# Kernel optimization log

Measured on AMD Instinct MI355X. Metric: run time of the kernel, lower is better.

The kernel has to match this reference:

```python
import jax, jax.numpy as jnp
import numpy as np

B, N, D, DC, R = 32, 36, 2048, 4, 512  # batch, regions, feat dim, coord dim, fusion rank


def setup_inputs() -> dict:
    key = jax.random.key(0)
    ks = jax.random.split(key, 8)
    s = lambda fan_in: 1.0 / np.sqrt(fan_in)
    return {
        "mm": jax.random.normal(ks[0], (B, N, D), dtype=jnp.float32),
        "coords": jax.random.uniform(ks[1], (B, N, DC), dtype=jnp.float32),
        "U_feat": jax.random.normal(ks[2], (D, R), dtype=jnp.float32) * s(D),
        "V_feat": jax.random.normal(ks[3], (D, R), dtype=jnp.float32) * s(D),
        "P_feat": jax.random.normal(ks[4], (R, D), dtype=jnp.float32) * s(R),
        "U_coord": jax.random.normal(ks[5], (DC, R), dtype=jnp.float32) * s(DC),
        "V_coord": jax.random.normal(ks[6], (DC, R), dtype=jnp.float32) * s(DC),
        "P_coord": jax.random.normal(ks[7], (R, D), dtype=jnp.float32) * s(R),
    }


def reference(mm, coords, U_feat, V_feat, P_feat, U_coord, V_coord, P_coord):
    # Pairwise module: build all (i, j) region pairs, fuse, max-aggregate over j.
    # Original torch code detach_()'s the gathered pair tensors -> stop_gradient here.
    mm_sg = jax.lax.stop_gradient(mm)
    coords_sg = jax.lax.stop_gradient(coords)

    # Coord fusion (MLB-style low-rank multiplicative fusion)
    uc = jnp.einsum("bnc,cr->bnr", coords_sg, U_coord)   # [B,N,R]
    vc = jnp.einsum("bnc,cr->bnr", coords_sg, V_coord)   # [B,N,R]
    zc = jax.nn.relu(uc[:, :, None, :] * vc[:, None, :, :])  # [B,N,N,R]
    Rij = jnp.einsum("bijr,rd->bijd", zc, P_coord)       # [B,N,N,D]

    # Feature fusion
    uf = jnp.einsum("bnd,dr->bnr", mm_sg, U_feat)
    vf = jnp.einsum("bnd,dr->bnr", mm_sg, V_feat)
    zf = jax.nn.relu(uf[:, :, None, :] * vf[:, None, :, :])  # [B,N,N,R]
    Rij = Rij + jnp.einsum("bijr,rd->bijd", zf, P_feat)  # [B,N,N,D]

    # agg['type'] == 'max': reduce over the second region axis (j)
    mm_new = jnp.max(Rij, axis=2)                        # [B,N,D]

    # residual
    return mm_new + mm
```

## Files before the change

### kernel.cpp

```cpp
#include <hip/hip_runtime.h>

#define BI    1152
#define NREG  36
#define DD    2048
#define RR    512
#define KK    1024
#define ZROWS (BI*NREG)
#define MBLK  144
#define NBLK  256
#define ABUF  (MBLK*32)
#define BBUF  (NBLK*32)
#define BUFE  (ABUF+BBUF)

typedef __bf16 bf16;
typedef __bf16 bf16x8 __attribute__((ext_vector_type(8)));
typedef __bf16 bf16x4 __attribute__((ext_vector_type(4)));
typedef float  f32x4  __attribute__((ext_vector_type(4)));

__device__ __forceinline__ void gl_lds16(const void* g, void* l) {
  __builtin_amdgcn_global_load_lds(
      (const __attribute__((address_space(1))) unsigned int*)g,
      (__attribute__((address_space(3))) unsigned int*)l, 16, 0, 0);
}

__global__ void k_prep(const float* __restrict__ mm, const float* __restrict__ coords,
                       const float* __restrict__ U_feat, const float* __restrict__ V_feat,
                       const float* __restrict__ P_feat, const float* __restrict__ U_coord,
                       const float* __restrict__ V_coord, const float* __restrict__ P_coord,
                       bf16* __restrict__ mmb, bf16* __restrict__ UT, bf16* __restrict__ VT,
                       bf16* __restrict__ PTt, float* __restrict__ uc, float* __restrict__ vc) {
  __shared__ float tile[32][33];
  int bid = blockIdx.x, tid = threadIdx.x;
  if (bid < 2304) {
    int i = bid * 256 + tid;
    float4 v = ((const float4*)mm)[i];
    bf16x4 o = {(bf16)v.x, (bf16)v.y, (bf16)v.z, (bf16)v.w};
    ((bf16x4*)mmb)[i] = o;
  } else if (bid < 4352) {
    int rel = bid - 2304;
    int zz = rel >> 10, rr = rel & 1023;
    int c0 = (rr & 15) * 32, r0 = (rr >> 4) * 32;
    const float* in = zz ? V_feat : U_feat;
    bf16* outp = zz ? VT : UT;
    int tx = tid & 31, ty = tid >> 5;
#pragma unroll
    for (int k = 0; k < 4; k++)
      tile[ty + 8 * k][tx] = in[(long)(r0 + ty + 8 * k) * 512 + c0 + tx];
    __syncthreads();
#pragma unroll
    for (int k = 0; k < 4; k++)
      outp[(long)(c0 + ty + 8 * k) * 2048 + r0 + tx] = (bf16)tile[tx][ty + 8 * k];
  } else if (bid < 6400) {
    int rel = bid - 4352;
    int zz = rel >> 10, rr = rel & 1023;
    int c0 = (rr & 63) * 32, r0 = (rr >> 6) * 32;
    const float* in = zz ? P_feat : P_coord;
    int koff = zz * 512;
    int tx = tid & 31, ty = tid >> 5;
#pragma unroll
    for (int k = 0; k < 4; k++)
      tile[ty + 8 * k][tx] = in[(long)(r0 + ty + 8 * k) * 2048 + c0 + tx];
    __syncthreads();
    int kc = (koff + r0) >> 5;
#pragma unroll
    for (int k = 0; k < 4; k++) {
      int d = c0 + ty + 8 * k;
      PTt[((long)kc * 2048 + d) * 32 + tx] = (bf16)tile[tx][ty + 8 * k];
    }
  } else {
    int g = bid - 6400;
    float c0 = coords[g * 4 + 0], c1 = coords[g * 4 + 1];
    float c2 = coords[g * 4 + 2], c3 = coords[g * 4 + 3];
#pragma unroll
    for (int i = 0; i < 2; i++) {
      int r = tid + i * 256;
      uc[g * RR + r] = c0 * U_coord[r] + c1 * U_coord[RR + r] + c2 * U_coord[2 * RR + r] + c3 * U_coord[3 * RR + r];
      vc[g * RR + r] = c0 * V_coord[r] + c1 * V_coord[RR + r] + c2 * V_coord[2 * RR + r] + c3 * V_coord[3 * RR + r];
    }
  }
}

__launch_bounds__(256)
__global__ void k_gemm_uv(const bf16* __restrict__ mmb, const bf16* __restrict__ UT,
                          const bf16* __restrict__ VT, float* __restrict__ uf,
                          float* __restrict__ vf, float* __restrict__ uf2,
                          float* __restrict__ vf2) {
  __shared__ bf16 lds2[2][6144];
  int uv = blockIdx.z >> 1, kh = blockIdx.z & 1;
  const bf16* Bmat = uv ? VT : UT;
  float* outp = uv ? (kh ? vf2 : vf) : (kh ? uf2 : uf);
  int m0 = blockIdx.x * 64, n0 = blockIdx.y * 128;
  int kbase = kh * 1024;
  int tid = threadIdx.x, wave = tid >> 6, lane = tid & 63;
  int l15 = lane & 15, qv = lane >> 4;
  int qp_c = qv ^ ((l15 >> 1) & 3);
  int qs = (lane & 3) ^ ((lane >> 3) & 3);

  const bf16* gA = mmb + (long)(m0 + wave * 16 + (lane >> 2)) * 2048 + kbase + qs * 8;
  const bf16* gB = Bmat + (long)(n0 + wave * 32 + (lane >> 2)) * 2048 + kbase + qs * 8;
  int lA = wave * 512;
  int lB = 2048 + wave * 1024;

  auto stage = [&](int buf, int k0) {
    bf16* db = &lds2[buf][0];
    gl_lds16(gA + k0, db + lA);
    gl_lds16(gB + k0, db + lB);
    gl_lds16(gB + 16 * 2048 + k0, db + lB + 512);
  };

  f32x4 acc[4][2] = {};
  stage(0, 0);
  for (int k0 = 0; k0 < 1024; k0 += 32) {
    int cur = (k0 >> 5) & 1;
    __syncthreads();
    if (k0 + 32 < 1024) stage(cur ^ 1, k0 + 32);
    bf16x8 a[4], b[2];
#pragma unroll
    for (int mt = 0; mt < 4; mt++)
      a[mt] = *(const bf16x8*)(&lds2[cur][0] + (mt * 16 + l15) * 32 + qp_c * 8);
#pragma unroll
    for (int nt = 0; nt < 2; nt++)
      b[nt] = *(const bf16x8*)(&lds2[cur][2048] + (wave * 32 + nt * 16 + l15) * 32 + qp_c * 8);
#pragma unroll
    for (int mt = 0; mt < 4; mt++)
#pragma unroll
      for (int nt = 0; nt < 2; nt++)
        acc[mt][nt] = __builtin_amdgcn_mfma_f32_16x16x32_bf16(a[mt], b[nt], acc[mt][nt], 0, 0, 0);
  }
#pragma unroll
  for (int mt = 0; mt < 4; mt++)
#pragma unroll
    for (int nt = 0; nt < 2; nt++)
#pragma unroll
      for (int r = 0; r < 4; r++) {
        int row = m0 + mt * 16 + qv * 4 + r;
        int col = n0 + wave * 32 + nt * 16 + l15;
        outp[(long)row * RR + col] = acc[mt][nt][r];
      }
}

__global__ void k_build_z(const float* __restrict__ uc, const float* __restrict__ vc,
                          const float* __restrict__ uf, const float* __restrict__ vf,
                          const float* __restrict__ uf2, const float* __restrict__ vf2,
                          bf16* __restrict__ z) {
  __shared__ float uL[36 * 128];
  __shared__ float vL[36 * 128];
  int kq = blockIdx.x, b = blockIdx.y, tid = threadIdx.x;
  int kb = (kq & 3) * 128;
  for (int i = tid; i < 1152; i += 256) {
    int row = i >> 5, kk = (i & 31) * 4;
    long src = (long)(b * 36 + row) * RR + kb + kk;
    float4 u4, v4;
    if (kq < 4) {
      u4 = *(const float4*)(uc + src);
      v4 = *(const float4*)(vc + src);
    } else {
      float4 a1 = *(const float4*)(uf + src), a2 = *(const float4*)(uf2 + src);
      float4 b1 = *(const float4*)(vf + src), b2 = *(const float4*)(vf2 + src);
      u4.x = a1.x + a2.x; u4.y = a1.y + a2.y; u4.z = a1.z + a2.z; u4.w = a1.w + a2.w;
      v4.x = b1.x + b2.x; v4.y = b1.y + b2.y; v4.z = b1.z + b2.z; v4.w = b1.w + b2.w;
    }
    *(float4*)&uL[row * 128 + kk] = u4;
    *(float4*)&vL[row * 128 + kk] = v4;
  }
  __syncthreads();
  int cbase = blockIdx.z * 20736;
  for (int c = cbase + tid; c < cbase + 20736; c += 256) {
    int kcl = c / 10368;
    int rem = c - kcl * 10368;
    int row = rem >> 3;
    int x4 = rem & 7;
    int gl = row / 36;
    int j = row - gl * 36;
    int kl = kcl * 32 + x4 * 4;
    float4 u4 = *(const float4*)&uL[gl * 128 + kl];
    float4 v4 = *(const float4*)&vL[j * 128 + kl];
    float x0 = fmaxf(u4.x * v4.x, 0.f), x1 = fmaxf(u4.y * v4.y, 0.f);
    float x2 = fmaxf(u4.z * v4.z, 0.f), x3 = fmaxf(u4.w * v4.w, 0.f);
    bf16x4 o = {(bf16)x0, (bf16)x1, (bf16)x2, (bf16)x3};
    int bi = b * 36 + gl;
    long rowp = (long)(bi >> 2) * 144 + j * 4 + (bi & 3);
    *(bf16x4*)(z + ((long)(kq * 4 + kcl) * ZROWS + rowp) * 32 + x4 * 4) = o;
  }
}

__launch_bounds__(256, 2)
__global__ void k_main(const bf16* __restrict__ z, const bf16* __restrict__ PTt,
                       const float* __restrict__ mm, float* __restrict__ out) {
  __shared__ bf16 lds[2 * BUFE];
  int bid = blockIdx.x;
  int x = bid & 7, t = bid >> 3;
  int dt = t & 7, go = (t >> 3) * 8 + x;
  int d0 = dt * NBLK;
  int tid = threadIdx.x, wave = tid >> 6, lane = tid & 63;
  int l15 = lane & 15, qv = lane >> 4;
  int qp_c = qv ^ ((l15 >> 1) & 3);
  int qs = (lane & 3) ^ ((lane >> 3) & 3);
  int lroff = (lane >> 2) * 32 + qs * 8;

  const bf16* gA = z + (long)go * ABUF + wave * 1024 + lroff;
  const bf16* gB = PTt + (long)d0 * 32 + wave * 2048 + lroff;
  int lA = wave * 1024;
  int lB = ABUF + wave * 2048;

  int sbuf = 0;
  auto stage = [&]() {
    bf16* db = lds + sbuf * BUFE;
    gl_lds16(gA, db + lA);
    gl_lds16(gA + 512, db + lA + 512);
    if (wave == 0) gl_lds16(gA + 4096, db + 4096);
    gl_lds16(gB, db + lB);
    gl_lds16(gB + 512, db + lB + 512);
    gl_lds16(gB + 1024, db + lB + 1024);
    gl_lds16(gB + 1536, db + lB + 1536);
    gA += (long)ZROWS * 32;
    gB += 2048L * 32;
    sbuf ^= 1;
  };

  f32x4 acc[9][4] = {};
  stage();
  for (int kc = 0; kc < 32; kc++) {
    __syncthreads();
    if (kc < 31) stage();
    const bf16* cur = lds + (kc & 1) * BUFE;
    bf16x8 b[4];
#pragma unroll
    for (int nt = 0; nt < 4; nt++)
      b[nt] = *(const bf16x8*)(cur + ABUF + (wave * 64 + nt * 16 + l15) * 32 + qp_c * 8);
#pragma unroll
    for (int mt = 0; mt < 9; mt++) {
      bf16x8 av = *(const bf16x8*)(cur + (mt * 16 + l15) * 32 + qp_c * 8);
#pragma unroll
      for (int nt = 0; nt < 4; nt++)
        acc[mt][nt] = __builtin_amdgcn_mfma_f32_16x16x32_bf16(av, b[nt], acc[mt][nt], 0, 0, 0);
    }
  }

#pragma unroll
  for (int nt = 0; nt < 4; nt++) {
    float mx[4];
#pragma unroll
    for (int r = 0; r < 4; r++) {
      mx[r] = acc[0][nt][r];
#pragma unroll
      for (int mt = 1; mt < 9; mt++) mx[r] = fmaxf(mx[r], acc[mt][nt][r]);
      mx[r] = fmaxf(mx[r], __shfl_xor(mx[r], 16, 64));
      mx[r] = fmaxf(mx[r], __shfl_xor(mx[r], 32, 64));
    }
    if (lane < 16) {
      int col = d0 + wave * 64 + nt * 16 + lane;
#pragma unroll
      for (int r = 0; r < 4; r++) {
        long oa = (long)(go * 4 + r) * DD + col;
        out[oa] = mx[r] + mm[oa];
      }
    }
  }
}

extern "C" void kernel_launch(void* const* d_in, const int* in_sizes, int n_in,
                              void* d_out, int out_size, void* d_ws, size_t ws_size,
                              hipStream_t stream) {
  const float* mm     = (const float*)d_in[0];
  const float* coords = (const float*)d_in[1];
  const float* U_feat = (const float*)d_in[2];
  const float* V_feat = (const float*)d_in[3];
  const float* P_feat = (const float*)d_in[4];
  const float* U_coord= (const float*)d_in[5];
  const float* V_coord= (const float*)d_in[6];
  const float* P_coord= (const float*)d_in[7];
  float* out = (float*)d_out;

  char* ws = (char*)d_ws;
  bf16* z   = (bf16*)(ws + 0);
  bf16* PTt = (bf16*)(ws + 84934656);
  bf16* mmb = (bf16*)(ws + 89128960);
  bf16* UT  = (bf16*)(ws + 93847552);
  bf16* VT  = (bf16*)(ws + 95944704);
  float* uf = (float*)(ws + 98041856);
  float* vf = (float*)(ws + 100401152);
  float* uc = (float*)(ws + 102760448);
  float* vc = (float*)(ws + 105119744);
  float* uf2= (float*)(ws + 107479040);
  float* vf2= (float*)(ws + 109838336);

  k_prep<<<dim3(7552), dim3(256), 0, stream>>>(mm, coords, U_feat, V_feat, P_feat,
                                               U_coord, V_coord, P_coord,
                                               mmb, UT, VT, PTt, uc, vc);
  k_gemm_uv<<<dim3(18, 4, 4), dim3(256), 0, stream>>>(mmb, UT, VT, uf, vf, uf2, vf2);
  k_build_z<<<dim3(8, 32, 2), dim3(256), 0, stream>>>(uc, vc, uf, vf, uf2, vf2, z);
  k_main<<<dim3(2304), dim3(256), 0, stream>>>(z, PTt, mm, out);
}
```

Baseline: 247.4 us.

## Triple-buffer main GEMM pipeline with explicit vmcnt waits and split uv GEMM 4-way

Changes the main fused GEMM from double to triple buffering in LDS, prefetching two K-chunks ahead. It replaces __syncthreads with manual s_waitcnt vmcnt plus s_barrier so one stage of loads stays in flight during compute. It also raises the split-K of the uv projection GEMM from 2 to 4 for more parallelism, summing the four partials in the z-building kernel. The cost is more LDS per block, which may limit occupancy, and extra partial-sum traffic.

```diff
diff --git a/kernel.cpp b/kernel.cpp
--- a/kernel.cpp
+++ b/kernel.cpp
@@ -82,15 +82,14 @@
 
 __launch_bounds__(256)
 __global__ void k_gemm_uv(const bf16* __restrict__ mmb, const bf16* __restrict__ UT,
-                          const bf16* __restrict__ VT, float* __restrict__ uf,
-                          float* __restrict__ vf, float* __restrict__ uf2,
-                          float* __restrict__ vf2) {
+                          const bf16* __restrict__ VT, float* __restrict__ ufp,
+                          float* __restrict__ vfp) {
   __shared__ bf16 lds2[2][6144];
-  int uv = blockIdx.z >> 1, kh = blockIdx.z & 1;
+  int uv = blockIdx.z >> 2, kh = blockIdx.z & 3;
   const bf16* Bmat = uv ? VT : UT;
-  float* outp = uv ? (kh ? vf2 : vf) : (kh ? uf2 : uf);
+  float* outp = (uv ? vfp : ufp) + (long)kh * (BI * RR);
   int m0 = blockIdx.x * 64, n0 = blockIdx.y * 128;
-  int kbase = kh * 1024;
+  int kbase = kh * 512;
   int tid = threadIdx.x, wave = tid >> 6, lane = tid & 63;
   int l15 = lane & 15, qv = lane >> 4;
   int qp_c = qv ^ ((l15 >> 1) & 3);
@@ -110,10 +109,10 @@
 
   f32x4 acc[4][2] = {};
   stage(0, 0);
-  for (int k0 = 0; k0 < 1024; k0 += 32) {
+  for (int k0 = 0; k0 < 512; k0 += 32) {
     int cur = (k0 >> 5) & 1;
     __syncthreads();
-    if (k0 + 32 < 1024) stage(cur ^ 1, k0 + 32);
+    if (k0 + 32 < 512) stage(cur ^ 1, k0 + 32);
     bf16x8 a[4], b[2];
 #pragma unroll
     for (int mt = 0; mt < 4; mt++)
@@ -140,8 +139,7 @@
 }
 
 __global__ void k_build_z(const float* __restrict__ uc, const float* __restrict__ vc,
-                          const float* __restrict__ uf, const float* __restrict__ vf,
-                          const float* __restrict__ uf2, const float* __restrict__ vf2,
+                          const float* __restrict__ ufp, const float* __restrict__ vfp,
                           bf16* __restrict__ z) {
   __shared__ float uL[36 * 128];
   __shared__ float vL[36 * 128];
@@ -155,10 +153,15 @@
       u4 = *(const float4*)(uc + src);
       v4 = *(const float4*)(vc + src);
     } else {
-      float4 a1 = *(const float4*)(uf + src), a2 = *(const float4*)(uf2 + src);
-      float4 b1 = *(const float4*)(vf + src), b2 = *(const float4*)(vf2 + src);
-      u4.x = a1.x + a2.x; u4.y = a1.y + a2.y; u4.z = a1.z + a2.z; u4.w = a1.w + a2.w;
-      v4.x = b1.x + b2.x; v4.y = b1.y + b2.y; v4.z = b1.z + b2.z; v4.w = b1.w + b2.w;
+      u4 = make_float4(0.f, 0.f, 0.f, 0.f);
+      v4 = make_float4(0.f, 0.f, 0.f, 0.f);
+#pragma unroll
+      for (int p = 0; p < 4; p++) {
+        float4 a1 = *(const float4*)(ufp + (long)p * (BI * RR) + src);
+        float4 b1 = *(const float4*)(vfp + (long)p * (BI * RR) + src);
+        u4.x += a1.x; u4.y += a1.y; u4.z += a1.z; u4.w += a1.w;
+        v4.x += b1.x; v4.y += b1.y; v4.z += b1.z; v4.w += b1.w;
+      }
     }
     *(float4*)&uL[row * 128 + kk] = u4;
     *(float4*)&vL[row * 128 + kk] = v4;
@@ -187,7 +190,7 @@
 __launch_bounds__(256, 2)
 __global__ void k_main(const bf16* __restrict__ z, const bf16* __restrict__ PTt,
                        const float* __restrict__ mm, float* __restrict__ out) {
-  __shared__ bf16 lds[2 * BUFE];
+  __shared__ bf16 lds[3 * BUFE];
   int bid = blockIdx.x;
   int x = bid & 7, t = bid >> 3;
   int dt = t & 7, go = (t >> 3) * 8 + x;
@@ -203,27 +206,35 @@
   int lA = wave * 1024;
   int lB = ABUF + wave * 2048;
 
-  int sbuf = 0;
-  auto stage = [&]() {
-    bf16* db = lds + sbuf * BUFE;
-    gl_lds16(gA, db + lA);
-    gl_lds16(gA + 512, db + lA + 512);
-    if (wave == 0) gl_lds16(gA + 4096, db + 4096);
-    gl_lds16(gB, db + lB);
-    gl_lds16(gB + 512, db + lB + 512);
-    gl_lds16(gB + 1024, db + lB + 1024);
-    gl_lds16(gB + 1536, db + lB + 1536);
-    gA += (long)ZROWS * 32;
-    gB += 2048L * 32;
-    sbuf ^= 1;
+  auto stage = [&](int buf, int kc) {
+    bf16* db = lds + buf * BUFE;
+    long ka = (long)kc * (ZROWS * 32L);
+    long kb = (long)kc * (2048L * 32);
+    gl_lds16(gA + ka, db + lA);
+    gl_lds16(gA + ka + 512, db + lA + 512);
+    if (wave == 3) gl_lds16(gA + ka + 1024, db + lA + 1024);
+    gl_lds16(gB + kb, db + lB);
+    gl_lds16(gB + kb + 512, db + lB + 512);
+    gl_lds16(gB + kb + 1024, db + lB + 1024);
+    gl_lds16(gB + kb + 1536, db + lB + 1536);
   };
 
   f32x4 acc[9][4] = {};
-  stage();
+  stage(0, 0);
+  stage(1, 1);
+  int buf = 0;
   for (int kc = 0; kc < 32; kc++) {
-    __syncthreads();
-    if (kc < 31) stage();
-    const bf16* cur = lds + (kc & 1) * BUFE;
+    if (kc < 31) {
+      if (wave == 3) __asm__ volatile("s_waitcnt vmcnt(7)\n\ts_barrier" ::: "memory");
+      else           __asm__ volatile("s_waitcnt vmcnt(6)\n\ts_barrier" ::: "memory");
+    } else {
+      __asm__ volatile("s_waitcnt vmcnt(0)\n\ts_barrier" ::: "memory");
+    }
+    if (kc + 2 < 32) {
+      int bnext = buf + 2; if (bnext >= 3) bnext -= 3;
+      stage(bnext, kc + 2);
+    }
+    const bf16* cur = lds + buf * BUFE;
     bf16x8 b[4];
 #pragma unroll
     for (int nt = 0; nt < 4; nt++)
@@ -235,6 +246,7 @@
       for (int nt = 0; nt < 4; nt++)
         acc[mt][nt] = __builtin_amdgcn_mfma_f32_16x16x32_bf16(av, b[nt], acc[mt][nt], 0, 0, 0);
     }
+    buf++; if (buf >= 3) buf -= 3;
   }
 
 #pragma unroll
@@ -278,17 +290,15 @@
   bf16* mmb = (bf16*)(ws + 89128960);
   bf16* UT  = (bf16*)(ws + 93847552);
   bf16* VT  = (bf16*)(ws + 95944704);
-  float* uf = (float*)(ws + 98041856);
-  float* vf = (float*)(ws + 100401152);
-  float* uc = (float*)(ws + 102760448);
-  float* vc = (float*)(ws + 105119744);
-  float* uf2= (float*)(ws + 107479040);
-  float* vf2= (float*)(ws + 109838336);
+  float* ufp= (float*)(ws + 98041856);
+  float* vfp= (float*)(ws + 107479040);
+  float* uc = (float*)(ws + 116916224);
+  float* vc = (float*)(ws + 119275520);
 
   k_prep<<<dim3(7552), dim3(256), 0, stream>>>(mm, coords, U_feat, V_feat, P_feat,
                                                U_coord, V_coord, P_coord,
                                                mmb, UT, VT, PTt, uc, vc);
-  k_gemm_uv<<<dim3(18, 4, 4), dim3(256), 0, stream>>>(mmb, UT, VT, uf, vf, uf2, vf2);
-  k_build_z<<<dim3(8, 32, 2), dim3(256), 0, stream>>>(uc, vc, uf, vf, uf2, vf2, z);
+  k_gemm_uv<<<dim3(18, 4, 8), dim3(256), 0, stream>>>(mmb, UT, VT, ufp, vfp);
+  k_build_z<<<dim3(8, 32, 2), dim3(256), 0, stream>>>(uc, vc, ufp, vfp, z);
   k_main<<<dim3(2304), dim3(256), 0, stream>>>(z, PTt, mm, out);
 }
```

New measurement: 254.3 us. +2.8%, slower.
